# Optimization experiments

Measured on AMD Instinct MI355X. Metric: run time of the kernel, lower is better.

## Reference

```python
import jax, jax.numpy as jnp
import numpy as np

KE_CONST = 14.3996
NUM_GRAPHS = 48
LONG_RANGE_SCALE = 1.0
SQRT2 = 1.41421356  # literal used in the torch jit script


def setup_inputs() -> dict:
    key = jax.random.key(0)
    ks = jax.random.split(key, 10)
    N, F = 6144, 128
    h0 = jax.random.normal(ks[0], (N, F), dtype=jnp.float32)
    h1 = jax.random.normal(ks[1], (N, F), dtype=jnp.float32)
    pos = jax.random.uniform(ks[2], (N, 3), dtype=jnp.float32) * 10.0  # atoms in a ~10A box
    batch = jnp.sort(jax.random.randint(ks[3], (N,), 0, NUM_GRAPHS))
    # q_proj params: Linear(F,F) + SiLU + Linear(F,1,bias=False), init normal(0,0.2)
    q_W1 = jax.random.normal(ks[4], (F, F), dtype=jnp.float32) * 0.2
    q_b1 = jnp.zeros((F,), dtype=jnp.float32)
    q_W2 = jax.random.normal(ks[5], (F, 1), dtype=jnp.float32) * 0.2
    sigma = jnp.asarray(1.0, dtype=jnp.float32)
    # vdw_proj params: Linear(F,F) + SiLU + Linear(F,2)
    s = 1.0 / np.sqrt(F)
    v_W1 = jax.random.normal(ks[6], (F, F), dtype=jnp.float32) * s
    v_b1 = jnp.zeros((F,), dtype=jnp.float32)
    v_W2 = jax.random.normal(ks[7], (F, 2), dtype=jnp.float32) * s
    v_b2 = jnp.zeros((2,), dtype=jnp.float32)
    return {"h0": h0, "h1": h1, "pos": pos, "q_W1": q_W1, "q_b1": q_b1,
            "q_W2": q_W2, "sigma": sigma, "v_W1": v_W1, "v_b1": v_b1,
            "v_W2": v_W2, "v_b2": v_b2, "batch": batch}


def _forward(h0, pos, q_W1, q_b1, q_W2, sigma, v_W1, v_b1, v_W2, v_b2, batch):
    N = h0.shape[0]
    dt = h0.dtype
    # --- charge head: q = Linear(SiLU(Linear(h0))) , per-graph mean-centered ---
    q = jax.nn.silu(h0 @ q_W1 + q_b1) @ q_W2  # [N,1]
    q_sum = jax.ops.segment_sum(q, batch, num_segments=NUM_GRAPHS)  # [G,1]
    counts = jax.ops.segment_sum(jnp.ones((N, 1), dt), batch, num_segments=NUM_GRAPHS)
    q_mean = q_sum / jnp.clip(counts, 1.0)
    q = q - q_mean[batch]
    # --- vdW head: c6, r_vdw = softplus(Linear(SiLU(Linear(h0)))) ---
    vdw_params = jax.nn.silu(h0 @ v_W1 + v_b1) @ v_W2 + v_b2  # [N,2]
    c6 = jax.nn.softplus(vdw_params[:, 0:1])     # [N,1]
    r_vdw = jax.nn.softplus(vdw_params[:, 1:2])  # [N,1]
    # --- dense pairwise geometry (non-periodic branch: cell is None) ---
    diff = pos[:, None, :] - pos[None, :, :]        # [N,N,3]
    dist_sq = jnp.sum(diff * diff, axis=-1)          # [N,N]
    dist = jnp.sqrt(dist_sq + 1e-8)
    batch_mask = batch[:, None] == batch[None, :]
    diag = jnp.eye(N, dtype=bool)
    mask = (batch_mask & ~diag).astype(dt)           # [N,N]
    # --- erf-shielded direct electrostatics ---
    qq = q @ q.T                                     # [N,N]
    shielding = jax.scipy.special.erf(dist / (SQRT2 * sigma))
    e_elec = 0.5 * KE_CONST * jnp.sum(qq * (1.0 / (dist + 1e-8)) * shielding * mask)
    # --- BJ-damped vdW ---
    c6_ij = jnp.sqrt(c6 @ c6.T)
    rvdw_ij = jnp.sqrt(r_vdw @ r_vdw.T)
    damping = dist_sq ** 3 + rvdw_ij ** 6
    e_vdw = 0.5 * jnp.sum(-(c6_ij / (damping + 1e-8)) * mask)
    return (e_elec + e_vdw) * LONG_RANGE_SCALE


def reference(h0, h1, pos, q_W1, q_b1, q_W2, sigma, v_W1, v_b1, v_W2, v_b2, batch):
    # h1 is accepted by the torch forward signature but unused on this path
    return _forward(h0, pos, q_W1, q_b1, q_W2, sigma, v_W1, v_b1, v_W2, v_b2, batch)
```

## Files before the change

kernel.cpp:

```cpp
#include <hip/hip_runtime.h>
#include <math.h>

#define NUM_GRAPHS 48
#define F 128
#define MB 16
#define SLICES 32
#define NPART (NUM_GRAPHS * SLICES)

__device__ __forceinline__ float softplus_f(float x) {
    return fmaxf(x, 0.0f) + log1pf(expf(-fabsf(x)));
}
__device__ __forceinline__ float silu_f(float x) {
    return x / (1.0f + expf(-x));
}

__global__ void seg_kernel(const int* __restrict__ batch, int* __restrict__ seg, int N) {
    int i = blockIdx.x * blockDim.x + threadIdx.x;
    if (i >= N) return;
    int b = batch[i];
    int prev = (i == 0) ? -1 : batch[i - 1];
    for (int g = prev + 1; g <= b; ++g) seg[g] = i;
    if (i == N - 1) {
        for (int g = b + 1; g <= NUM_GRAPHS; ++g) seg[g] = N;
    }
}

__global__ __launch_bounds__(256) void mlp_kernel(
    const float* __restrict__ h0,
    const float* __restrict__ qW1, const float* __restrict__ qb1,
    const float* __restrict__ qW2,
    const float* __restrict__ vW1, const float* __restrict__ vb1,
    const float* __restrict__ vW2, const float* __restrict__ vb2,
    float* __restrict__ q_raw, float* __restrict__ c6, float* __restrict__ rv,
    int N)
{
    __shared__ float h0s[MB][F];
    __shared__ float red[4][8][3];
    const int tid = threadIdx.x;
    const int a0 = blockIdx.x * MB;

    for (int idx = tid; idx < MB * (F / 4); idx += 256) {
        int a = idx >> 5;
        int kq = idx & 31;
        int row = a0 + a;
        float4 v = make_float4(0.f, 0.f, 0.f, 0.f);
        if (row < N) v = ((const float4*)(h0 + (size_t)row * F))[kq];
        ((float4*)&h0s[a][0])[kq] = v;
    }
    __syncthreads();

    const int j  = tid & 127;
    const int g2 = tid >> 7;

    float accq[8], accv[8];
    const float qb = qb1[j], vb = vb1[j];
    #pragma unroll
    for (int a = 0; a < 8; ++a) { accq[a] = qb; accv[a] = vb; }

    const float* __restrict__ qc = qW1 + j;
    const float* __restrict__ vc = vW1 + j;

    #pragma unroll 2
    for (int k4 = 0; k4 < F / 4; ++k4) {
        float wq[4], wv[4];
        #pragma unroll
        for (int u = 0; u < 4; ++u) {
            wq[u] = qc[(size_t)(k4 * 4 + u) * F];
            wv[u] = vc[(size_t)(k4 * 4 + u) * F];
        }
        #pragma unroll
        for (int a = 0; a < 8; ++a) {
            float4 hv = ((const float4*)&h0s[g2 * 8 + a][0])[k4];
            float tq = accq[a];
            tq = fmaf(hv.x, wq[0], tq);
            tq = fmaf(hv.y, wq[1], tq);
            tq = fmaf(hv.z, wq[2], tq);
            tq = fmaf(hv.w, wq[3], tq);
            accq[a] = tq;
            float tv = accv[a];
            tv = fmaf(hv.x, wv[0], tv);
            tv = fmaf(hv.y, wv[1], tv);
            tv = fmaf(hv.z, wv[2], tv);
            tv = fmaf(hv.w, wv[3], tv);
            accv[a] = tv;
        }
    }

    const float w2q = qW2[j];
    const float w20 = vW2[2 * j];
    const float w21 = vW2[2 * j + 1];
    const int wave = tid >> 6;

    #pragma unroll
    for (int a = 0; a < 8; ++a) {
        float pq = silu_f(accq[a]) * w2q;
        float sv = silu_f(accv[a]);
        float p0 = sv * w20;
        float p1 = sv * w21;
        #pragma unroll
        for (int d = 32; d >= 1; d >>= 1) {
            pq += __shfl_xor(pq, d);
            p0 += __shfl_xor(p0, d);
            p1 += __shfl_xor(p1, d);
        }
        if ((tid & 63) == 0) {
            red[wave][a][0] = pq;
            red[wave][a][1] = p0;
            red[wave][a][2] = p1;
        }
    }
    __syncthreads();

    if (tid < MB) {
        int g  = tid >> 3;
        int al = tid & 7;
        int row = a0 + tid;
        if (row < N) {
            float pq = red[2 * g][al][0] + red[2 * g + 1][al][0];
            float p0 = red[2 * g][al][1] + red[2 * g + 1][al][1];
            float p1 = red[2 * g][al][2] + red[2 * g + 1][al][2];
            q_raw[row] = pq;
            c6[row] = softplus_f(p0 + vb2[0]);
            rv[row] = softplus_f(p1 + vb2[1]);
        }
    }
}

__global__ __launch_bounds__(64) void pair_kernel(
    const float* __restrict__ pos,
    const float* __restrict__ q_raw,
    const float* __restrict__ c6a, const float* __restrict__ rva,
    const int* __restrict__ seg, const float* __restrict__ sigma_p,
    float* __restrict__ part)
{
    int g     = blockIdx.x / SLICES;
    int slice = blockIdx.x % SLICES;
    int lane  = threadIdx.x;
    int s0 = seg[g], s1 = seg[g + 1];
    int n = s1 - s0;
    float acc = 0.0f;
    if (n > 0) {
        float ms = 0.f;
        for (int i = s0 + lane; i < s1; i += 64) ms += q_raw[i];
        #pragma unroll
        for (int d = 32; d >= 1; d >>= 1) ms += __shfl_xor(ms, d);
        float mean = ms / fmaxf((float)n, 1.0f);
        float inv_ss = 1.0f / (1.41421356f * sigma_p[0]);
        for (int i = s0 + slice; i < s1; i += SLICES) {
            float xi = pos[3*i+0], yi = pos[3*i+1], zi = pos[3*i+2];
            float qi  = q_raw[i] - mean;
            float c6i = c6a[i];
            float rvi = rva[i];
            for (int jj = s0 + lane; jj < s1; jj += 64) {
                if (jj == i) continue;
                float dx = xi - pos[3*jj+0];
                float dy = yi - pos[3*jj+1];
                float dz = zi - pos[3*jj+2];
                float d2 = fmaf(dx, dx, fmaf(dy, dy, dz * dz));
                float dist = sqrtf(d2 + 1e-8f);
                float qj = q_raw[jj] - mean;
                float e1 = qi * qj * erff(dist * inv_ss) / (dist + 1e-8f);
                float c6ij = sqrtf(c6i * c6a[jj]);
                float rr   = rvi * rva[jj];
                float damp = fmaf(d2 * d2, d2, rr * rr * rr);
                float e2 = c6ij / (damp + 1e-8f);
                acc += (0.5f * 14.3996f) * e1 - 0.5f * e2;
            }
        }
    }
    #pragma unroll
    for (int d = 32; d >= 1; d >>= 1) acc += __shfl_xor(acc, d);
    if (lane == 0) part[blockIdx.x] = acc;
}

__global__ __launch_bounds__(256) void finalize_kernel(
    const float* __restrict__ part, int nparts, float* __restrict__ out)
{
    __shared__ double reds[4];
    int tid = threadIdx.x;
    double s = 0.0;
    for (int i = tid; i < nparts; i += 256) s += (double)part[i];
    #pragma unroll
    for (int d = 32; d >= 1; d >>= 1) s += __shfl_xor(s, d);
    if ((tid & 63) == 0) reds[tid >> 6] = s;
    __syncthreads();
    if (tid == 0) {
        double t = reds[0] + reds[1] + reds[2] + reds[3];
        out[0] = (float)t;
    }
}

extern "C" void kernel_launch(void* const* d_in, const int* in_sizes, int n_in,
                              void* d_out, int out_size, void* d_ws, size_t ws_size,
                              hipStream_t stream) {
    const float* h0   = (const float*)d_in[0];
    const float* pos  = (const float*)d_in[2];
    const float* qW1  = (const float*)d_in[3];
    const float* qb1  = (const float*)d_in[4];
    const float* qW2  = (const float*)d_in[5];
    const float* sig  = (const float*)d_in[6];
    const float* vW1  = (const float*)d_in[7];
    const float* vb1  = (const float*)d_in[8];
    const float* vW2  = (const float*)d_in[9];
    const float* vb2  = (const float*)d_in[10];
    const int*  batch = (const int*)d_in[11];
    const int N = in_sizes[0] / F;

    char* ws = (char*)d_ws;
    int*   seg   = (int*)ws;
    float* part  = (float*)(ws + 256);
    float* q_raw = (float*)(ws + 256 + NPART * 4);
    float* c6    = q_raw + N;
    float* rv    = c6 + N;
    float* out   = (float*)d_out;

    seg_kernel<<<(N + 255) / 256, 256, 0, stream>>>(batch, seg, N);
    mlp_kernel<<<(N + MB - 1) / MB, 256, 0, stream>>>(
        h0, qW1, qb1, qW2, vW1, vb1, vW2, vb2, q_raw, c6, rv, N);
    pair_kernel<<<NPART, 64, 0, stream>>>(pos, q_raw, c6, rv, seg, sig, part);
    finalize_kernel<<<1, 256, 0, stream>>>(part, NPART, out);
}
```

Measured before the change: 118.4 us.

## Stage pair-kernel atoms in shared memory, precompute sqrt(c6)/r^3, fuse segment setup

```diff
diff --git a/kernel.cpp b/kernel.cpp
--- a/kernel.cpp
+++ b/kernel.cpp
@@ -4,25 +4,15 @@
 #define NUM_GRAPHS 48
 #define F 128
 #define MB 16
-#define SLICES 32
-#define NPART (NUM_GRAPHS * SLICES)
+#define R 8
+#define NPB (NUM_GRAPHS * R)
+#define CHUNK 512
 
 __device__ __forceinline__ float softplus_f(float x) {
     return fmaxf(x, 0.0f) + log1pf(expf(-fabsf(x)));
 }
 __device__ __forceinline__ float silu_f(float x) {
     return x / (1.0f + expf(-x));
-}
-
-__global__ void seg_kernel(const int* __restrict__ batch, int* __restrict__ seg, int N) {
-    int i = blockIdx.x * blockDim.x + threadIdx.x;
-    if (i >= N) return;
-    int b = batch[i];
-    int prev = (i == 0) ? -1 : batch[i - 1];
-    for (int g = prev + 1; g <= b; ++g) seg[g] = i;
-    if (i == N - 1) {
-        for (int g = b + 1; g <= NUM_GRAPHS; ++g) seg[g] = N;
-    }
 }
 
 __global__ __launch_bounds__(256) void mlp_kernel(
@@ -31,13 +21,25 @@
     const float* __restrict__ qW2,
     const float* __restrict__ vW1, const float* __restrict__ vb1,
     const float* __restrict__ vW2, const float* __restrict__ vb2,
-    float* __restrict__ q_raw, float* __restrict__ c6, float* __restrict__ rv,
+    const int* __restrict__ batch, int* __restrict__ seg,
+    float* __restrict__ q_raw, float* __restrict__ c6s, float* __restrict__ rv3,
     int N)
 {
     __shared__ float h0s[MB][F];
     __shared__ float red[4][8][3];
     const int tid = threadIdx.x;
     const int a0 = blockIdx.x * MB;
+
+    if (blockIdx.x == 0) {
+        for (int i = tid; i < N; i += 256) {
+            int b = batch[i];
+            int prev = (i == 0) ? -1 : batch[i - 1];
+            for (int g = prev + 1; g <= b; ++g) seg[g] = i;
+            if (i == N - 1) {
+                for (int g = b + 1; g <= NUM_GRAPHS; ++g) seg[g] = N;
+            }
+        }
+    }
 
     for (int idx = tid; idx < MB * (F / 4); idx += 256) {
         int a = idx >> 5;
@@ -60,13 +62,21 @@
     const float* __restrict__ qc = qW1 + j;
     const float* __restrict__ vc = vW1 + j;
 
+    float wq[4], wv[4];
+    #pragma unroll
+    for (int u = 0; u < 4; ++u) {
+        wq[u] = qc[(size_t)u * F];
+        wv[u] = vc[(size_t)u * F];
+    }
+
     #pragma unroll 2
     for (int k4 = 0; k4 < F / 4; ++k4) {
-        float wq[4], wv[4];
+        int kn = (k4 < F / 4 - 1) ? (k4 + 1) : k4;
+        float nq[4], nv[4];
         #pragma unroll
         for (int u = 0; u < 4; ++u) {
-            wq[u] = qc[(size_t)(k4 * 4 + u) * F];
-            wv[u] = vc[(size_t)(k4 * 4 + u) * F];
+            nq[u] = qc[(size_t)(kn * 4 + u) * F];
+            nv[u] = vc[(size_t)(kn * 4 + u) * F];
         }
         #pragma unroll
         for (int a = 0; a < 8; ++a) {
@@ -84,6 +94,8 @@
             tv = fmaf(hv.w, wv[3], tv);
             accv[a] = tv;
         }
+        #pragma unroll
+        for (int u = 0; u < 4; ++u) { wq[u] = nq[u]; wv[u] = nv[u]; }
     }
 
     const float w2q = qW2[j];
@@ -120,57 +132,85 @@
             float p0 = red[2 * g][al][1] + red[2 * g + 1][al][1];
             float p1 = red[2 * g][al][2] + red[2 * g + 1][al][2];
             q_raw[row] = pq;
-            c6[row] = softplus_f(p0 + vb2[0]);
-            rv[row] = softplus_f(p1 + vb2[1]);
-        }
-    }
-}
-
-__global__ __launch_bounds__(64) void pair_kernel(
+            c6s[row] = sqrtf(softplus_f(p0 + vb2[0]));
+            float r  = softplus_f(p1 + vb2[1]);
+            rv3[row] = r * r * r;
+        }
+    }
+}
+
+__global__ __launch_bounds__(256) void pair_kernel(
     const float* __restrict__ pos,
     const float* __restrict__ q_raw,
-    const float* __restrict__ c6a, const float* __restrict__ rva,
+    const float* __restrict__ c6s, const float* __restrict__ rv3,
     const int* __restrict__ seg, const float* __restrict__ sigma_p,
     float* __restrict__ part)
 {
-    int g     = blockIdx.x / SLICES;
-    int slice = blockIdx.x % SLICES;
-    int lane  = threadIdx.x;
-    int s0 = seg[g], s1 = seg[g + 1];
-    int n = s1 - s0;
+    __shared__ float xs[CHUNK], ys[CHUNK], zs[CHUNK];
+    __shared__ float qs[CHUNK], ss[CHUNK], r3[CHUNK];
+    __shared__ float wred[4];
+
+    const int g     = blockIdx.x / R;
+    const int slice = blockIdx.x % R;
+    const int tid   = threadIdx.x;
+    const int wave  = tid >> 6;
+    const int lane  = tid & 63;
+    const int s0 = seg[g], s1 = seg[g + 1];
+    const int n = s1 - s0;
+
     float acc = 0.0f;
-    if (n > 0) {
+    if (n > 1) {
         float ms = 0.f;
         for (int i = s0 + lane; i < s1; i += 64) ms += q_raw[i];
         #pragma unroll
         for (int d = 32; d >= 1; d >>= 1) ms += __shfl_xor(ms, d);
-        float mean = ms / fmaxf((float)n, 1.0f);
-        float inv_ss = 1.0f / (1.41421356f * sigma_p[0]);
-        for (int i = s0 + slice; i < s1; i += SLICES) {
-            float xi = pos[3*i+0], yi = pos[3*i+1], zi = pos[3*i+2];
-            float qi  = q_raw[i] - mean;
-            float c6i = c6a[i];
-            float rvi = rva[i];
-            for (int jj = s0 + lane; jj < s1; jj += 64) {
-                if (jj == i) continue;
-                float dx = xi - pos[3*jj+0];
-                float dy = yi - pos[3*jj+1];
-                float dz = zi - pos[3*jj+2];
-                float d2 = fmaf(dx, dx, fmaf(dy, dy, dz * dz));
-                float dist = sqrtf(d2 + 1e-8f);
-                float qj = q_raw[jj] - mean;
-                float e1 = qi * qj * erff(dist * inv_ss) / (dist + 1e-8f);
-                float c6ij = sqrtf(c6i * c6a[jj]);
-                float rr   = rvi * rva[jj];
-                float damp = fmaf(d2 * d2, d2, rr * rr * rr);
-                float e2 = c6ij / (damp + 1e-8f);
-                acc += (0.5f * 14.3996f) * e1 - 0.5f * e2;
+        const float mean = ms / (float)n;
+        const float inv_ss = 1.0f / (1.41421356f * sigma_p[0]);
+        const int wv = slice * 4 + wave;
+
+        for (int c0 = s0; c0 < s1; c0 += CHUNK) {
+            const int cn = min(CHUNK, s1 - c0);
+            __syncthreads();
+            for (int idx = tid; idx < cn; idx += 256) {
+                int a = c0 + idx;
+                xs[idx] = pos[3 * a + 0];
+                ys[idx] = pos[3 * a + 1];
+                zs[idx] = pos[3 * a + 2];
+                qs[idx] = q_raw[a] - mean;
+                ss[idx] = c6s[a];
+                r3[idx] = rv3[a];
             }
+            __syncthreads();
+
+            for (int i = s0 + wv; i < s1; i += 4 * R) {
+                float xi = pos[3 * i + 0], yi = pos[3 * i + 1], zi = pos[3 * i + 2];
+                float qi = q_raw[i] - mean;
+                float si = c6s[i];
+                float ri = rv3[i];
+                for (int jd = lane; jd < cn; jd += 64) {
+                    if (c0 + jd == i) continue;
+                    float dx = xi - xs[jd];
+                    float dy = yi - ys[jd];
+                    float dz = zi - zs[jd];
+                    float d2 = fmaf(dx, dx, fmaf(dy, dy, dz * dz));
+                    float dist = sqrtf(d2 + 1e-8f);
+                    float e1 = qi * qs[jd] * erff(dist * inv_ss) / (dist + 1e-8f);
+                    float damp = fmaf(d2 * d2, d2, fmaf(ri, r3[jd], 1e-8f));
+                    float e2 = si * ss[jd] / damp;
+                    acc += (0.5f * 14.3996f) * e1 - 0.5f * e2;
+                }
+            }
         }
     }
     #pragma unroll
     for (int d = 32; d >= 1; d >>= 1) acc += __shfl_xor(acc, d);
-    if (lane == 0) part[blockIdx.x] = acc;
+    if (n > 1) {
+        if (lane == 0) wred[wave] = acc;
+        __syncthreads();
+        if (tid == 0) part[blockIdx.x] = wred[0] + wred[1] + wred[2] + wred[3];
+    } else if (tid == 0) {
+        part[blockIdx.x] = 0.0f;
+    }
 }
 
 __global__ __launch_bounds__(256) void finalize_kernel(
@@ -184,10 +224,7 @@
     for (int d = 32; d >= 1; d >>= 1) s += __shfl_xor(s, d);
     if ((tid & 63) == 0) reds[tid >> 6] = s;
     __syncthreads();
-    if (tid == 0) {
-        double t = reds[0] + reds[1] + reds[2] + reds[3];
-        out[0] = (float)t;
-    }
+    if (tid == 0) out[0] = (float)(reds[0] + reds[1] + reds[2] + reds[3]);
 }
 
 extern "C" void kernel_launch(void* const* d_in, const int* in_sizes, int n_in,
@@ -209,14 +246,13 @@
     char* ws = (char*)d_ws;
     int*   seg   = (int*)ws;
     float* part  = (float*)(ws + 256);
-    float* q_raw = (float*)(ws + 256 + NPART * 4);
-    float* c6    = q_raw + N;
-    float* rv    = c6 + N;
+    float* q_raw = (float*)(ws + 256 + NPB * 4);
+    float* c6s   = q_raw + N;
+    float* rv3   = c6s + N;
     float* out   = (float*)d_out;
 
-    seg_kernel<<<(N + 255) / 256, 256, 0, stream>>>(batch, seg, N);
     mlp_kernel<<<(N + MB - 1) / MB, 256, 0, stream>>>(
-        h0, qW1, qb1, qW2, vW1, vb1, vW2, vb2, q_raw, c6, rv, N);
-    pair_kernel<<<NPART, 64, 0, stream>>>(pos, q_raw, c6, rv, seg, sig, part);
-    finalize_kernel<<<1, 256, 0, stream>>>(part, NPART, out);
-}
+        h0, qW1, qb1, qW2, vW1, vb1, vW2, vb2, batch, seg, q_raw, c6s, rv3, N);
+    pair_kernel<<<NPB, 256, 0, stream>>>(pos, q_raw, c6s, rv3, seg, sig, part);
+    finalize_kernel<<<1, 256, 0, stream>>>(part, NPB, out);
+}
```

Result: faster. 110.1 us (-7.0%).
